# Optimization experiments

Hardware: AMD Instinct MI355X
Metric: run time of the kernel (lower is better)

## Reference

```python
import jax, jax.numpy as jnp
import numpy as np

B, S, D, E = 8, 128, 768, 100

def setup_inputs() -> dict:
    key = jax.random.key(0)
    ks = jax.random.split(key, 7)
    s = 1.0 / np.sqrt(D)  # roughly Linear init scale
    return {
        "x":     jax.random.normal(ks[0], (B, S, D), dtype=jnp.float32),
        "w_lin": jax.random.normal(ks[1], (E, D, D), dtype=jnp.float32) * s,
        "b_lin": jax.random.normal(ks[2], (E, D), dtype=jnp.float32) * s,
        "w1":    jax.random.normal(ks[3], (E, D, D), dtype=jnp.float32) * s,
        "b1":    jax.random.normal(ks[4], (E, D), dtype=jnp.float32) * s,
        "w2":    jax.random.normal(ks[5], (E, D, D), dtype=jnp.float32) * s,
        "b2":    jax.random.normal(ks[6], (E, D), dtype=jnp.float32) * s,
    }

def reference(x, w_lin, b_lin, w1, b1, w2, b2):
    # Torch Linear: y = x @ W.T + b, weights stacked over experts e.
    # Skip branch: [B,S,O,E]
    lin = jnp.einsum('bsd,eod->bsoe', x, w_lin) + b_lin.T[None, None]
    # MLP branch (dropout is identity in eval mode); exact (erf) GELU as nn.GELU default.
    h = jax.nn.gelu(jnp.einsum('bsd,ehd->bseh', x, w1) + b1[None, None], approximate=False)
    mlp = jnp.einsum('bseh,eoh->bsoe', h, w2) + b2.T[None, None]
    # torch.stack([...], dim=-1) -> [B, S, D_out, E]
    return lin + mlp
```

## Files before the change

### kernel.cpp

```cpp
#include <hip/hip_runtime.h>
#include <hip/hip_bf16.h>
#include <cstdint>

typedef __attribute__((ext_vector_type(8))) short short8;
typedef __attribute__((ext_vector_type(4))) float f32x4;
typedef unsigned short u16;
typedef unsigned int u32;

#define Mdim 1024
#define Ddim 768
#define Edim 100
#define DD (Ddim * Ddim)

__device__ __forceinline__ u16 f2bf(float f) {
  u32 u = __builtin_bit_cast(u32, f);
  u += 0x7fffu + ((u >> 16) & 1u);
  return (u16)(u >> 16);
}
__device__ __forceinline__ float bf2f(u16 h) {
  return __builtin_bit_cast(float, ((u32)h) << 16);
}
__device__ __forceinline__ u32 pack2(float a, float b) {
  return (u32)f2bf(a) | ((u32)f2bf(b) << 16);
}

__device__ __forceinline__ float gelu_f(float v) {
  float v2 = v * v;
  float wv = v * (2.30220795f + 0.10294322f * v2);
  float ew = __builtin_amdgcn_exp2f(wv);
  return v - v * __builtin_amdgcn_rcpf(ew + 1.0f);
}

#define GLL16(gsrc, ldst)                                                        \
  __builtin_amdgcn_global_load_lds(                                             \
      (const __attribute__((address_space(1))) u32*)(gsrc),                     \
      (__attribute__((address_space(3))) u32*)(ldst), 16, 0, 0)

#define VM8 asm volatile("s_waitcnt vmcnt(8)" ::: "memory")
#define VM0 asm volatile("s_waitcnt vmcnt(0)" ::: "memory")
#define LGKM0 asm volatile("s_waitcnt lgkmcnt(0)" ::: "memory")
#define RAW_BAR                                                                  \
  do {                                                                           \
    __builtin_amdgcn_s_barrier();                                                \
    asm volatile("" ::: "memory");                                               \
  } while (0)

__global__ void k_cvt(const float* __restrict__ x, u16* __restrict__ xb) {
  size_t i = ((size_t)blockIdx.x * 256 + threadIdx.x) * 4;
  float4 v = *(const float4*)(x + i);
  uint2 r;
  r.x = pack2(v.x, v.y);
  r.y = pack2(v.z, v.w);
  *(uint2*)(xb + i) = r;
}

__global__ __launch_bounds__(256) void k_cvtw(const float* __restrict__ w,
                                              u16* __restrict__ wb, int n8) {
  const int stride = gridDim.x * 256;
  for (int i = blockIdx.x * 256 + threadIdx.x; i < n8; i += stride) {
    const size_t o = (size_t)i * 8;
    const float4 f0 = *(const float4*)(w + o);
    const float4 f1 = *(const float4*)(w + o + 4);
    uint4 v;
    v.x = pack2(f0.x, f0.y); v.y = pack2(f0.z, f0.w);
    v.z = pack2(f1.x, f1.y); v.w = pack2(f1.z, f1.w);
    *(uint4*)(wb + o) = v;
  }
}

template <int NT>
__device__ __forceinline__ void gemm8(const u16* __restrict__ A0,
                                      const u16* __restrict__ A1,
                                      const u16* __restrict__ B0,
                                      const u16* __restrict__ B1,
                                      u16* lds, f32x4 (&acc)[8][4], const int t) {
  const int w = t >> 6, l = t & 63;
  const int wr = (w >> 2) << 7;
  const int wc = (w & 3) << 6;
  const int lr = l & 15, c4 = l >> 4, r7 = l & 7;
  const int sl0 = ((c4 ^ r7) << 3);
  const int sl1 = (((4 | c4) ^ r7) << 3);
  const size_t soff = (size_t)((w << 5) + (l >> 3)) * Ddim + (((l & 7) ^ (l >> 3)) << 3);

  auto stage_op = [&](const u16* src, int buf, int isB, int kk) {
    u16* d = lds + (buf << 15) + (isB << 14) + (w << 11);
    const u16* s = src + soff + (kk << 6);
#pragma unroll
    for (int i = 0; i < 4; ++i)
      GLL16(s + (size_t)(i << 3) * Ddim, d + (i << 9));
  };
  auto stage = [&](int tt, int isB) {
    const int buf = tt & 1;
    if (NT == 24 && tt >= 12) stage_op(isB ? B1 : A1, buf, isB, tt - 12);
    else                      stage_op(isB ? B0 : A0, buf, isB, tt);
  };

  short8 af[16], bf[4];
  auto rdA = [&](int buf, int half) {
    const u16* ab = lds + (buf << 15) + (wr + (half << 6) + lr) * 64;
#pragma unroll
    for (int m = 0; m < 4; ++m) {
      af[half * 8 + m * 2]     = *(const short8*)(ab + (m << 10) + sl0);
      af[half * 8 + m * 2 + 1] = *(const short8*)(ab + (m << 10) + sl1);
    }
  };
  auto rdB = [&](int buf, int half) {
    const u16* bb = lds + (buf << 15) + 16384 + (wc + (half << 5) + lr) * 64;
#pragma unroll
    for (int n = 0; n < 2; ++n) {
      bf[n * 2]     = *(const short8*)(bb + (n << 10) + sl0);
      bf[n * 2 + 1] = *(const short8*)(bb + (n << 10) + sl1);
    }
  };
  auto q = [&](int mh, int nh) {
    __builtin_amdgcn_s_setprio(1);
#pragma unroll
    for (int m = 0; m < 4; ++m)
#pragma unroll
      for (int n = 0; n < 2; ++n) {
        f32x4 c = acc[mh * 4 + m][nh * 2 + n];
        c = __builtin_amdgcn_mfma_f32_16x16x32_bf16(af[mh * 8 + m * 2],     bf[n * 2],     c, 0, 0, 0);
        c = __builtin_amdgcn_mfma_f32_16x16x32_bf16(af[mh * 8 + m * 2 + 1], bf[n * 2 + 1], c, 0, 0, 0);
        acc[mh * 4 + m][nh * 2 + n] = c;
      }
    __builtin_amdgcn_s_setprio(0);
  };

  stage(0, 1); stage(0, 0);
  stage(1, 1); stage(1, 0);
  VM8;
  RAW_BAR;

#pragma unroll 2
  for (int T = 0; T < NT - 2; ++T) {
    const int buf = T & 1;
    rdA(buf, 0); rdB(buf, 0);
    RAW_BAR; q(0, 0); RAW_BAR;
    rdA(buf, 1);
    RAW_BAR; q(1, 0); RAW_BAR;
    rdB(buf, 1); stage(T + 2, 0);
    RAW_BAR; q(1, 1); RAW_BAR;
    stage(T + 2, 1);
    VM8;
    RAW_BAR; q(0, 1); RAW_BAR;
  }
  {
    const int buf = (NT - 2) & 1;
    rdA(buf, 0); rdB(buf, 0); RAW_BAR; q(0, 0); RAW_BAR;
    rdA(buf, 1);              RAW_BAR; q(1, 0); RAW_BAR;
    rdB(buf, 1);              RAW_BAR; q(1, 1); RAW_BAR;
    VM0; RAW_BAR; q(0, 1); RAW_BAR;
  }
  {
    const int buf = (NT - 1) & 1;
    rdA(buf, 0); rdB(buf, 0); RAW_BAR; q(0, 0); RAW_BAR;
    rdA(buf, 1);              RAW_BAR; q(1, 0); RAW_BAR;
    rdB(buf, 1);              RAW_BAR; q(1, 1); RAW_BAR;
    q(0, 1);
  }
}

template <bool GELU>
__device__ __forceinline__ void epi_store(f32x4 (&acc)[8][4], const float* bias,
                                          u16* lds, u16* gout, int m_base, int n_base,
                                          const int t) {
  const int w = t >> 6, l = t & 63;
  const int lr = l & 15, c4 = l >> 4;
  u16* reg = lds + (w << 13);

  LGKM0;
  __builtin_amdgcn_sched_barrier(0);
  RAW_BAR;

  float bv[4];
#pragma unroll
  for (int nf = 0; nf < 4; ++nf) bv[nf] = bias[(nf << 4) + lr];

#pragma unroll
  for (int mf = 0; mf < 8; ++mf) {
#pragma unroll
    for (int nf = 0; nf < 4; ++nf) {
      const int slot = (nf << 1) + (lr >> 3);
      const int bis = (lr & 7);
#pragma unroll
      for (int j = 0; j < 4; ++j) {
        float v = acc[mf][nf][j] + bv[nf];
        if (GELU) v = gelu_f(v);
        const int row = (mf << 4) + (c4 << 2) + j;
        reg[row * 64 + ((slot ^ (row & 7)) << 3) + bis] = f2bf(v);
      }
    }
  }
  const int g = l >> 3;
  const int phys = ((l & 7) ^ g) << 3;
#pragma unroll
  for (int r = 0; r < 16; ++r) {
    const int row = (r << 3) + g;
    short8 v = *(const short8*)(reg + row * 64 + phys);
    *(short8*)(gout + (size_t)(m_base + row) * Ddim + n_base + ((l & 7) << 3)) = v;
  }
}

__device__ __forceinline__ void decode8(int bid, int& e, int& m0, int& n0) {
  const int s = (bid & 7) * 150 + (bid >> 3);
  e = s / 12;
  const int r = s % 12;
  m0 = (r & 3) << 8;
  n0 = (r >> 2) << 8;
}

__global__ __launch_bounds__(512, 2) void k_h6(const u16* __restrict__ xb,
                                               const u16* __restrict__ w1b,
                                               const float* __restrict__ b1,
                                               u16* __restrict__ hout) {
  __shared__ __align__(16) u16 lds[65536];
  int e, m0, n0;
  decode8(blockIdx.x, e, m0, n0);
  const int t = threadIdx.x;
  f32x4 acc[8][4] = {};
  gemm8<12>(xb + (size_t)m0 * Ddim, nullptr,
            w1b + (size_t)e * DD + (size_t)n0 * Ddim, nullptr, lds, acc, t);

  const int w = t >> 6;
  const int wr = (w >> 2) << 7, wc = (w & 3) << 6;
  epi_store<true>(acc, b1 + (size_t)e * Ddim + n0 + wc, lds,
                  hout + (size_t)e * Mdim * Ddim, m0 + wr, n0 + wc, t);
}

__global__ __launch_bounds__(512, 2) void k_out6(const u16* __restrict__ xb,
                                                 const u16* __restrict__ hbuf,
                                                 const u16* __restrict__ wlb,
                                                 const float* __restrict__ b_lin,
                                                 const u16* __restrict__ w2b,
                                                 const float* __restrict__ b2,
                                                 u16* __restrict__ tout) {
  __shared__ __align__(16) u16 lds[65536];
  int e, m0, n0;
  decode8(blockIdx.x, e, m0, n0);
  const int t = threadIdx.x;
  f32x4 acc[8][4] = {};
  gemm8<24>(xb + (size_t)m0 * Ddim,
            hbuf + (size_t)e * Mdim * Ddim + (size_t)m0 * Ddim,
            wlb + (size_t)e * DD + (size_t)n0 * Ddim,
            w2b + (size_t)e * DD + (size_t)n0 * Ddim, lds, acc, t);

  const int w = t >> 6, l = t & 63;
  const int wr = (w >> 2) << 7, wc = (w & 3) << 6;
  const int lr = l & 15;
  const float* bm = b2 + (size_t)e * Ddim + n0 + wc;
#pragma unroll
  for (int nf = 0; nf < 4; ++nf) {
    const float bmv = bm[(nf << 4) + lr];
#pragma unroll
    for (int mf = 0; mf < 8; ++mf)
#pragma unroll
      for (int j = 0; j < 4; ++j) acc[mf][nf][j] += bmv;
  }
  epi_store<false>(acc, b_lin + (size_t)e * Ddim + n0 + wc, lds,
                   tout + (size_t)e * Mdim * Ddim, m0 + wr, n0 + wc, t);
}

__global__ __launch_bounds__(256) void k_tr_bf(const u16* __restrict__ tbuf,
                                               float* __restrict__ out) {
  __shared__ __align__(16) u16 tile[100 * 260];
  const int t = threadIdx.x;
  const size_t MD = (size_t)Mdim * Ddim;
  const size_t md0 = (size_t)blockIdx.x * 256;
#pragma unroll
  for (int p = 0; p < 25; ++p) {
    const int e = p * 4 + (t >> 6);
    const int c = (t & 63) * 4;
    uint2 v = *(const uint2*)(tbuf + (size_t)e * MD + md0 + c);
    *(uint2*)(&tile[e * 260 + c]) = v;
  }
  __syncthreads();
  const size_t obase = md0 * 100;
#pragma unroll 5
  for (int i = 0; i < 100; ++i) {
    const int flat = t + i * 256;
    const int mo = (int)(((u32)flat * 5243u) >> 19);
    const int e = flat - mo * 100;
    out[obase + flat] = bf2f(tile[e * 260 + mo]);
  }
}

__device__ __forceinline__ void gemm_phase_f32(const u16* __restrict__ Ag,
                                               const float* __restrict__ Wg,
                                               u16* As, u16* Bs, f32x4 (&acc)[4][4], int t) {
  const int w = t >> 6, l = t & 63;
  const int lrow = l & 15, lk = (l >> 4) << 3;
  const int wr = ((w >> 1) << 6), wc = ((w & 1) << 6);
  for (int kt = 0; kt < Ddim; kt += 32) {
#pragma unroll
    for (int i = 0; i < 2; ++i) {
      GLL16(Ag + (size_t)((w << 5) + (i << 4) + (l >> 2)) * Ddim + kt + ((l & 3) << 3),
            As + (((w << 5) + (i << 4)) << 5));
    }
    {
      const int r = t >> 1, c = (t & 1) << 4;
      const float* src = Wg + (size_t)r * Ddim + kt + c;
      const float4 f0 = *(const float4*)(src);
      const float4 f1 = *(const float4*)(src + 4);
      const float4 f2 = *(const float4*)(src + 8);
      const float4 f3 = *(const float4*)(src + 12);
      uint4 v0, v1;
      v0.x = pack2(f0.x, f0.y); v0.y = pack2(f0.z, f0.w);
      v0.z = pack2(f1.x, f1.y); v0.w = pack2(f1.z, f1.w);
      v1.x = pack2(f2.x, f2.y); v1.y = pack2(f2.z, f2.w);
      v1.z = pack2(f3.x, f3.y); v1.w = pack2(f3.z, f3.w);
      *(uint4*)(&Bs[r * 32 + c]) = v0;
      *(uint4*)(&Bs[r * 32 + c + 8]) = v1;
    }
    __syncthreads();
    short8 af[4], bfr[4];
#pragma unroll
    for (int f = 0; f < 4; ++f) {
      af[f]  = *(const short8*)(&As[(wr + f * 16 + lrow) * 32 + lk]);
      bfr[f] = *(const short8*)(&Bs[(wc + f * 16 + lrow) * 32 + lk]);
    }
#pragma unroll
    for (int fm = 0; fm < 4; ++fm)
#pragma unroll
      for (int fn = 0; fn < 4; ++fn)
        acc[fm][fn] = __builtin_amdgcn_mfma_f32_16x16x32_bf16(af[fm], bfr[fn], acc[fm][fn], 0, 0, 0);
    __syncthreads();
  }
}

__global__ __launch_bounds__(256) void k_h2(const u16* __restrict__ xb,
                                            const float* __restrict__ w1,
                                            const float* __restrict__ b1,
                                            u16* __restrict__ hout, int e_base) {
  __shared__ __align__(16) u16 As[128 * 32];
  __shared__ __align__(16) u16 Bs[128 * 32];
  const int el = blockIdx.x / 48, r = blockIdx.x % 48;
  const int m0 = (r / 6) * 128, n0 = (r % 6) * 128;
  const int e = e_base + el;
  const int t = threadIdx.x, l = t & 63, wv = t >> 6;
  const int wr = (wv >> 1) * 64, wc = (wv & 1) * 64, lrow = l & 15;
  f32x4 acc[4][4] = {};
  gemm_phase_f32(xb + (size_t)m0 * Ddim, w1 + (size_t)e * DD + (size_t)n0 * Ddim, As, Bs, acc, t);
  const float* bias = b1 + (size_t)e * Ddim + n0;
  u16* hb = hout + (size_t)el * Mdim * Ddim;
#pragma unroll
  for (int fm = 0; fm < 4; ++fm) {
    const int mb = m0 + wr + fm * 16 + ((l >> 4) << 2);
#pragma unroll
    for (int fn = 0; fn < 4; ++fn) {
      const int nc = wc + fn * 16 + lrow;
      const float bv = bias[nc];
#pragma unroll
      for (int j = 0; j < 4; ++j) {
        float v = acc[fm][fn][j] + bv;
        v = 0.5f * v * (1.0f + erff(v * 0.7071067811865475f));
        hb[(size_t)(mb + j) * Ddim + n0 + nc] = f2bf(v);
      }
    }
  }
}

__global__ __launch_bounds__(256) void k_out2(
    const u16* __restrict__ xb, const u16* __restrict__ hbuf,
    const float* __restrict__ wl, const float* __restrict__ b_lin,
    const float* __restrict__ w2, const float* __restrict__ b2,
    float* __restrict__ out, int e_base) {
  __shared__ __align__(16) u16 As[128 * 32];
  __shared__ __align__(16) u16 Bs[128 * 32];
  const int el = blockIdx.x / 48, r = blockIdx.x % 48;
  const int m0 = (r / 6) * 128, n0 = (r % 6) * 128;
  const int e = e_base + el;
  const int t = threadIdx.x, l = t & 63, wv = t >> 6;
  const int wr = (wv >> 1) * 64, wc = (wv & 1) * 64, lrow = l & 15;
  f32x4 acc[4][4] = {};
  gemm_phase_f32(xb + (size_t)m0 * Ddim, wl + (size_t)e * DD + (size_t)n0 * Ddim, As, Bs, acc, t);
  gemm_phase_f32(hbuf + (size_t)el * Mdim * Ddim + (size_t)m0 * Ddim,
                 w2 + (size_t)e * DD + (size_t)n0 * Ddim, As, Bs, acc, t);
  const float* bl = b_lin + (size_t)e * Ddim + n0;
  const float* bm = b2 + (size_t)e * Ddim + n0;
#pragma unroll
  for (int fm = 0; fm < 4; ++fm) {
    const int mb = m0 + wr + fm * 16 + ((l >> 4) << 2);
#pragma unroll
    for (int fn = 0; fn < 4; ++fn) {
      const int nc = wc + fn * 16 + lrow;
      const float bv = bl[nc] + bm[nc];
#pragma unroll
      for (int j = 0; j < 4; ++j)
        out[((size_t)(mb + j) * Ddim + n0 + nc) * Edim + e] = acc[fm][fn][j] + bv;
    }
  }
}

extern "C" void kernel_launch(void* const* d_in, const int* in_sizes, int n_in,
                              void* d_out, int out_size, void* d_ws, size_t ws_size,
                              hipStream_t stream) {
  const float* x     = (const float*)d_in[0];
  const float* w_lin = (const float*)d_in[1];
  const float* b_lin = (const float*)d_in[2];
  const float* w1    = (const float*)d_in[3];
  const float* b1    = (const float*)d_in[4];
  const float* w2    = (const float*)d_in[5];
  const float* b2    = (const float*)d_in[6];
  float* out = (float*)d_out;

  const size_t MD = (size_t)Mdim * Ddim;
  const size_t xb_b   = MD * 2;
  const size_t w1_b   = (size_t)Edim * DD * 2;
  const size_t wreg_b = 2 * w1_b;
  const size_t h_b    = (size_t)Edim * MD * 2;
  const size_t tb_b   = h_b;
  const int NW8 = (int)((size_t)Edim * DD / 8);

  char* base = (char*)d_ws;
  u16* xb = (u16*)base;
  k_cvt<<<dim3((u32)(MD / 1024)), dim3(256), 0, stream>>>(x, xb);

  if (ws_size >= xb_b + wreg_b + h_b + tb_b) {
    u16* wreg = (u16*)(base + xb_b);
    u16* hbuf = (u16*)(base + xb_b + wreg_b);
    u16* tbuf = (u16*)(base + xb_b + wreg_b + h_b);
    k_cvtw<<<dim3(2048), dim3(256), 0, stream>>>(w1, wreg, NW8);
    k_h6<<<dim3(1200), dim3(512), 0, stream>>>(xb, wreg, b1, hbuf);
    k_cvtw<<<dim3(2048), dim3(256), 0, stream>>>(w_lin, wreg, NW8);
    k_cvtw<<<dim3(2048), dim3(256), 0, stream>>>(w2, wreg + (size_t)Edim * DD, NW8);
    k_out6<<<dim3(1200), dim3(512), 0, stream>>>(xb, hbuf, wreg, b_lin,
                                                 wreg + (size_t)Edim * DD, b2, tbuf);
    k_tr_bf<<<dim3((u32)(MD / 256)), dim3(256), 0, stream>>>(tbuf, out);
  } else {
    size_t avail = ws_size > xb_b ? ws_size - xb_b : 0;
    int EC = (int)(avail / (MD * 2));
    if (EC < 1) EC = 1;
    if (EC > Edim) EC = Edim;
    u16* hbuf = (u16*)(base + xb_b);
    for (int e0 = 0; e0 < Edim; e0 += EC) {
      int ne = (Edim - e0) < EC ? (Edim - e0) : EC;
      k_h2<<<dim3(ne * 48), dim3(256), 0, stream>>>(xb, w1, b1, hbuf, e0);
      k_out2<<<dim3(ne * 48), dim3(256), 0, stream>>>(xb, hbuf, w_lin, b_lin, w2, b2,
                                                      out, e0);
    }
  }
}
```

Before: 705.2 us.

## Fuse fp32 weight conversion into GEMM B-tile staging via register loads

Drops the separate weight-conversion kernels. The GEMMs now read fp32 weights directly: B tiles are loaded into registers, packed to bf16, and written to swizzled LDS, while A tiles still use direct global-to-LDS loads. The quarter order is also rearranged so A and B fragment registers can be reused. This removes an extra full pass over all weights (read fp32, write bf16, read bf16 again) and frees the weight workspace, at the cost of twice the global bytes per B tile inside the GEMM, higher register pressure, and B-tile LDS writes that are no longer asynchronous.

Measured after the change: 794.2 us. +12.6%, slower.

```diff
diff --git a/kernel.cpp b/kernel.cpp
--- a/kernel.cpp
+++ b/kernel.cpp
@@ -37,6 +37,7 @@
       (__attribute__((address_space(3))) u32*)(ldst), 16, 0, 0)
 
 #define VM8 asm volatile("s_waitcnt vmcnt(8)" ::: "memory")
+#define VM4 asm volatile("s_waitcnt vmcnt(4)" ::: "memory")
 #define VM0 asm volatile("s_waitcnt vmcnt(0)" ::: "memory")
 #define LGKM0 asm volatile("s_waitcnt lgkmcnt(0)" ::: "memory")
 #define RAW_BAR                                                                  \
@@ -54,109 +55,135 @@
   *(uint2*)(xb + i) = r;
 }
 
-__global__ __launch_bounds__(256) void k_cvtw(const float* __restrict__ w,
-                                              u16* __restrict__ wb, int n8) {
-  const int stride = gridDim.x * 256;
-  for (int i = blockIdx.x * 256 + threadIdx.x; i < n8; i += stride) {
-    const size_t o = (size_t)i * 8;
-    const float4 f0 = *(const float4*)(w + o);
-    const float4 f1 = *(const float4*)(w + o + 4);
-    uint4 v;
-    v.x = pack2(f0.x, f0.y); v.y = pack2(f0.z, f0.w);
-    v.z = pack2(f1.x, f1.y); v.w = pack2(f1.z, f1.w);
-    *(uint4*)(wb + o) = v;
-  }
-}
-
 template <int NT>
-__device__ __forceinline__ void gemm8(const u16* __restrict__ A0,
-                                      const u16* __restrict__ A1,
-                                      const u16* __restrict__ B0,
-                                      const u16* __restrict__ B1,
-                                      u16* lds, f32x4 (&acc)[8][4], const int t) {
+__device__ __forceinline__ void gemm8f(const u16* __restrict__ A0,
+                                       const u16* __restrict__ A1,
+                                       const float* __restrict__ B0,
+                                       const float* __restrict__ B1,
+                                       u16* lds, f32x4 (&acc)[8][4], const int t) {
   const int w = t >> 6, l = t & 63;
   const int wr = (w >> 2) << 7;
   const int wc = (w & 3) << 6;
   const int lr = l & 15, c4 = l >> 4, r7 = l & 7;
   const int sl0 = ((c4 ^ r7) << 3);
   const int sl1 = (((4 | c4) ^ r7) << 3);
-  const size_t soff = (size_t)((w << 5) + (l >> 3)) * Ddim + (((l & 7) ^ (l >> 3)) << 3);
-
-  auto stage_op = [&](const u16* src, int buf, int isB, int kk) {
-    u16* d = lds + (buf << 15) + (isB << 14) + (w << 11);
-    const u16* s = src + soff + (kk << 6);
+  const size_t soffA = (size_t)((w << 5) + (l >> 3)) * Ddim + (((l & 7) ^ (l >> 3)) << 3);
+  const size_t soffB = (size_t)((w << 5) + (l >> 3)) * Ddim + ((l & 7) << 3);
+  const int ldsB = ((w << 5) + (l >> 3)) * 64 + (((l & 7) ^ (l >> 3)) << 3);
+
+  auto stageA = [&](int tt) {
+    const u16* src = (NT == 24 && tt >= 12) ? A1 : A0;
+    const int kk = (NT == 24 && tt >= 12) ? tt - 12 : tt;
+    u16* d = lds + ((tt & 1) << 15) + (w << 11);
+    const u16* s = src + soffA + (kk << 6);
 #pragma unroll
     for (int i = 0; i < 4; ++i)
       GLL16(s + (size_t)(i << 3) * Ddim, d + (i << 9));
   };
-  auto stage = [&](int tt, int isB) {
-    const int buf = tt & 1;
-    if (NT == 24 && tt >= 12) stage_op(isB ? B1 : A1, buf, isB, tt - 12);
-    else                      stage_op(isB ? B0 : A0, buf, isB, tt);
-  };
-
-  short8 af[16], bf[4];
-  auto rdA = [&](int buf, int half) {
+  auto issueB = [&](int tt, uint4 (&br)[8]) {
+    const float* src = (NT == 24 && tt >= 12) ? B1 : B0;
+    const int kk = (NT == 24 && tt >= 12) ? tt - 12 : tt;
+    const float* s = src + soffB + (kk << 6);
+#pragma unroll
+    for (int i = 0; i < 4; ++i) {
+      br[i * 2]     = *(const uint4*)(s + (size_t)(i << 3) * Ddim);
+      br[i * 2 + 1] = *(const uint4*)(s + (size_t)(i << 3) * Ddim + 4);
+    }
+    asm volatile("" ::: "memory");
+  };
+  auto writeB = [&](int tt, uint4 (&br)[8]) {
+    u16* base = lds + ((tt & 1) << 15) + 16384 + ldsB;
+#pragma unroll
+    for (int i = 0; i < 4; ++i) {
+      const uint4 va = br[i * 2], vb = br[i * 2 + 1];
+      uint4 o;
+      o.x = pack2(__builtin_bit_cast(float, va.x), __builtin_bit_cast(float, va.y));
+      o.y = pack2(__builtin_bit_cast(float, va.z), __builtin_bit_cast(float, va.w));
+      o.z = pack2(__builtin_bit_cast(float, vb.x), __builtin_bit_cast(float, vb.y));
+      o.w = pack2(__builtin_bit_cast(float, vb.z), __builtin_bit_cast(float, vb.w));
+      *(uint4*)(base + (i << 3) * 64) = o;
+    }
+  };
+
+  auto rdA = [&](int buf, int half, short8 (&af)[8]) {
     const u16* ab = lds + (buf << 15) + (wr + (half << 6) + lr) * 64;
 #pragma unroll
     for (int m = 0; m < 4; ++m) {
-      af[half * 8 + m * 2]     = *(const short8*)(ab + (m << 10) + sl0);
-      af[half * 8 + m * 2 + 1] = *(const short8*)(ab + (m << 10) + sl1);
-    }
-  };
-  auto rdB = [&](int buf, int half) {
+      af[m * 2]     = *(const short8*)(ab + (m << 10) + sl0);
+      af[m * 2 + 1] = *(const short8*)(ab + (m << 10) + sl1);
+    }
+  };
+  auto rdB = [&](int buf, int half, short8 (&bfh)[4]) {
     const u16* bb = lds + (buf << 15) + 16384 + (wc + (half << 5) + lr) * 64;
 #pragma unroll
     for (int n = 0; n < 2; ++n) {
-      bf[n * 2]     = *(const short8*)(bb + (n << 10) + sl0);
-      bf[n * 2 + 1] = *(const short8*)(bb + (n << 10) + sl1);
-    }
-  };
-  auto q = [&](int mh, int nh) {
+      bfh[n * 2]     = *(const short8*)(bb + (n << 10) + sl0);
+      bfh[n * 2 + 1] = *(const short8*)(bb + (n << 10) + sl1);
+    }
+  };
+  auto q = [&](int mh, int nh, short8 (&af)[8], short8 (&bfh)[4]) {
     __builtin_amdgcn_s_setprio(1);
 #pragma unroll
     for (int m = 0; m < 4; ++m)
 #pragma unroll
       for (int n = 0; n < 2; ++n) {
         f32x4 c = acc[mh * 4 + m][nh * 2 + n];
-        c = __builtin_amdgcn_mfma_f32_16x16x32_bf16(af[mh * 8 + m * 2],     bf[n * 2],     c, 0, 0, 0);
-        c = __builtin_amdgcn_mfma_f32_16x16x32_bf16(af[mh * 8 + m * 2 + 1], bf[n * 2 + 1], c, 0, 0, 0);
+        c = __builtin_amdgcn_mfma_f32_16x16x32_bf16(af[m * 2],     bfh[n * 2],     c, 0, 0, 0);
+        c = __builtin_amdgcn_mfma_f32_16x16x32_bf16(af[m * 2 + 1], bfh[n * 2 + 1], c, 0, 0, 0);
         acc[mh * 4 + m][nh * 2 + n] = c;
       }
     __builtin_amdgcn_s_setprio(0);
   };
 
-  stage(0, 1); stage(0, 0);
-  stage(1, 1); stage(1, 0);
-  VM8;
-  RAW_BAR;
-
+  {
+    uint4 br0[8], br1[8];
+    issueB(0, br0); issueB(1, br1);
+    stageA(0); stageA(1);
+    VM8;
+    writeB(0, br0); writeB(1, br1);
+    VM4;
+    LGKM0;
+    RAW_BAR;
+  }
+
+  short8 afr[8], bf0[4], bf1[4];
+  uint4 br[8];
 #pragma unroll 2
   for (int T = 0; T < NT - 2; ++T) {
     const int buf = T & 1;
-    rdA(buf, 0); rdB(buf, 0);
-    RAW_BAR; q(0, 0); RAW_BAR;
-    rdA(buf, 1);
-    RAW_BAR; q(1, 0); RAW_BAR;
-    rdB(buf, 1); stage(T + 2, 0);
-    RAW_BAR; q(1, 1); RAW_BAR;
-    stage(T + 2, 1);
-    VM8;
-    RAW_BAR; q(0, 1); RAW_BAR;
+    issueB(T + 2, br);
+    rdA(buf, 0, afr); rdB(buf, 0, bf0);
+    RAW_BAR; q(0, 0, afr, bf0); RAW_BAR;
+    rdB(buf, 1, bf1);
+    RAW_BAR; q(0, 1, afr, bf1); RAW_BAR;
+    rdA(buf, 1, afr);
+    RAW_BAR; q(1, 1, afr, bf1); RAW_BAR;
+    stageA(T + 2);
+    writeB(T + 2, br);
+    VM4;
+    LGKM0;
+    RAW_BAR; q(1, 0, afr, bf0); RAW_BAR;
   }
   {
     const int buf = (NT - 2) & 1;
-    rdA(buf, 0); rdB(buf, 0); RAW_BAR; q(0, 0); RAW_BAR;
-    rdA(buf, 1);              RAW_BAR; q(1, 0); RAW_BAR;
-    rdB(buf, 1);              RAW_BAR; q(1, 1); RAW_BAR;
-    VM0; RAW_BAR; q(0, 1); RAW_BAR;
+    rdA(buf, 0, afr); rdB(buf, 0, bf0);
+    RAW_BAR; q(0, 0, afr, bf0); RAW_BAR;
+    rdB(buf, 1, bf1);
+    RAW_BAR; q(0, 1, afr, bf1); RAW_BAR;
+    rdA(buf, 1, afr);
+    RAW_BAR; q(1, 1, afr, bf1); RAW_BAR;
+    VM0;
+    RAW_BAR; q(1, 0, afr, bf0); RAW_BAR;
   }
   {
     const int buf = (NT - 1) & 1;
-    rdA(buf, 0); rdB(buf, 0); RAW_BAR; q(0, 0); RAW_BAR;
-    rdA(buf, 1);              RAW_BAR; q(1, 0); RAW_BAR;
-    rdB(buf, 1);              RAW_BAR; q(1, 1); RAW_BAR;
-    q(0, 1);
+    rdA(buf, 0, afr); rdB(buf, 0, bf0);
+    RAW_BAR; q(0, 0, afr, bf0); RAW_BAR;
+    rdB(buf, 1, bf1);
+    RAW_BAR; q(0, 1, afr, bf1); RAW_BAR;
+    rdA(buf, 1, afr);
+    RAW_BAR; q(1, 1, afr, bf1); RAW_BAR;
+    q(1, 0, afr, bf0);
   }
 }
 
@@ -209,8 +236,8 @@
   n0 = (r >> 2) << 8;
 }
 
-__global__ __launch_bounds__(512, 2) void k_h6(const u16* __restrict__ xb,
-                                               const u16* __restrict__ w1b,
+__global__ __launch_bounds__(512, 2) void k_h7(const u16* __restrict__ xb,
+                                               const float* __restrict__ w1,
                                                const float* __restrict__ b1,
                                                u16* __restrict__ hout) {
   __shared__ __align__(16) u16 lds[65536];
@@ -218,8 +245,8 @@
   decode8(blockIdx.x, e, m0, n0);
   const int t = threadIdx.x;
   f32x4 acc[8][4] = {};
-  gemm8<12>(xb + (size_t)m0 * Ddim, nullptr,
-            w1b + (size_t)e * DD + (size_t)n0 * Ddim, nullptr, lds, acc, t);
+  gemm8f<12>(xb + (size_t)m0 * Ddim, nullptr,
+             w1 + (size_t)e * DD + (size_t)n0 * Ddim, nullptr, lds, acc, t);
 
   const int w = t >> 6;
   const int wr = (w >> 2) << 7, wc = (w & 3) << 6;
@@ -227,11 +254,11 @@
                   hout + (size_t)e * Mdim * Ddim, m0 + wr, n0 + wc, t);
 }
 
-__global__ __launch_bounds__(512, 2) void k_out6(const u16* __restrict__ xb,
+__global__ __launch_bounds__(512, 2) void k_out7(const u16* __restrict__ xb,
                                                  const u16* __restrict__ hbuf,
-                                                 const u16* __restrict__ wlb,
+                                                 const float* __restrict__ wl,
                                                  const float* __restrict__ b_lin,
-                                                 const u16* __restrict__ w2b,
+                                                 const float* __restrict__ w2,
                                                  const float* __restrict__ b2,
                                                  u16* __restrict__ tout) {
   __shared__ __align__(16) u16 lds[65536];
@@ -239,10 +266,10 @@
   decode8(blockIdx.x, e, m0, n0);
   const int t = threadIdx.x;
   f32x4 acc[8][4] = {};
-  gemm8<24>(xb + (size_t)m0 * Ddim,
-            hbuf + (size_t)e * Mdim * Ddim + (size_t)m0 * Ddim,
-            wlb + (size_t)e * DD + (size_t)n0 * Ddim,
-            w2b + (size_t)e * DD + (size_t)n0 * Ddim, lds, acc, t);
+  gemm8f<24>(xb + (size_t)m0 * Ddim,
+             hbuf + (size_t)e * Mdim * Ddim + (size_t)m0 * Ddim,
+             wl + (size_t)e * DD + (size_t)n0 * Ddim,
+             w2 + (size_t)e * DD + (size_t)n0 * Ddim, lds, acc, t);
 
   const int w = t >> 6, l = t & 63;
   const int wr = (w >> 2) << 7, wc = (w & 3) << 6;
@@ -404,27 +431,19 @@
   float* out = (float*)d_out;
 
   const size_t MD = (size_t)Mdim * Ddim;
-  const size_t xb_b   = MD * 2;
-  const size_t w1_b   = (size_t)Edim * DD * 2;
-  const size_t wreg_b = 2 * w1_b;
-  const size_t h_b    = (size_t)Edim * MD * 2;
-  const size_t tb_b   = h_b;
-  const int NW8 = (int)((size_t)Edim * DD / 8);
+  const size_t xb_b = MD * 2;
+  const size_t h_b  = (size_t)Edim * MD * 2;
+  const size_t tb_b = h_b;
 
   char* base = (char*)d_ws;
   u16* xb = (u16*)base;
   k_cvt<<<dim3((u32)(MD / 1024)), dim3(256), 0, stream>>>(x, xb);
 
-  if (ws_size >= xb_b + wreg_b + h_b + tb_b) {
-    u16* wreg = (u16*)(base + xb_b);
-    u16* hbuf = (u16*)(base + xb_b + wreg_b);
-    u16* tbuf = (u16*)(base + xb_b + wreg_b + h_b);
-    k_cvtw<<<dim3(2048), dim3(256), 0, stream>>>(w1, wreg, NW8);
-    k_h6<<<dim3(1200), dim3(512), 0, stream>>>(xb, wreg, b1, hbuf);
-    k_cvtw<<<dim3(2048), dim3(256), 0, stream>>>(w_lin, wreg, NW8);
-    k_cvtw<<<dim3(2048), dim3(256), 0, stream>>>(w2, wreg + (size_t)Edim * DD, NW8);
-    k_out6<<<dim3(1200), dim3(512), 0, stream>>>(xb, hbuf, wreg, b_lin,
-                                                 wreg + (size_t)Edim * DD, b2, tbuf);
+  if (ws_size >= xb_b + h_b + tb_b) {
+    u16* hbuf = (u16*)(base + xb_b);
+    u16* tbuf = (u16*)(base + xb_b + h_b);
+    k_h7<<<dim3(1200), dim3(512), 0, stream>>>(xb, w1, b1, hbuf);
+    k_out7<<<dim3(1200), dim3(512), 0, stream>>>(xb, hbuf, w_lin, b_lin, w2, b2, tbuf);
     k_tr_bf<<<dim3((u32)(MD / 256)), dim3(256), 0, stream>>>(tbuf, out);
   } else {
     size_t avail = ws_size > xb_b ? ws_size - xb_b : 0;
```

## Fuse weight conversions into prep and first GEMM kernels to cut launches

Applied to the files above, without the earlier changes.

Merges the x and w1 bf16 conversions into a single prep kernel. It also moves the w_lin and w2 conversions into the tail of the first expert GEMM kernel, so they run inside that kernel instead of as separate launches. The aim is to drop kernel launches and let the conversion traffic overlap with GEMM tail work. The cost is a larger workspace (a third weight buffer) and GEMM blocks that run longer, with their conversion loops competing with other blocks' GEMM work for bandwidth.

After: 728.6 us. 3.3% more time.

```diff
diff --git a/kernel.cpp b/kernel.cpp
--- a/kernel.cpp
+++ b/kernel.cpp
@@ -11,6 +11,7 @@
 #define Ddim 768
 #define Edim 100
 #define DD (Ddim * Ddim)
+#define NW8 7372800
 
 __device__ __forceinline__ u16 f2bf(float f) {
   u32 u = __builtin_bit_cast(u32, f);
@@ -45,27 +46,23 @@
     asm volatile("" ::: "memory");                                               \
   } while (0)
 
-__global__ void k_cvt(const float* __restrict__ x, u16* __restrict__ xb) {
-  size_t i = ((size_t)blockIdx.x * 256 + threadIdx.x) * 4;
-  float4 v = *(const float4*)(x + i);
-  uint2 r;
-  r.x = pack2(v.x, v.y);
-  r.y = pack2(v.z, v.w);
-  *(uint2*)(xb + i) = r;
-}
-
-__global__ __launch_bounds__(256) void k_cvtw(const float* __restrict__ w,
-                                              u16* __restrict__ wb, int n8) {
-  const int stride = gridDim.x * 256;
-  for (int i = blockIdx.x * 256 + threadIdx.x; i < n8; i += stride) {
-    const size_t o = (size_t)i * 8;
-    const float4 f0 = *(const float4*)(w + o);
-    const float4 f1 = *(const float4*)(w + o + 4);
-    uint4 v;
-    v.x = pack2(f0.x, f0.y); v.y = pack2(f0.z, f0.w);
-    v.z = pack2(f1.x, f1.y); v.w = pack2(f1.z, f1.w);
-    *(uint4*)(wb + o) = v;
-  }
+__device__ __forceinline__ void cvt8(const float* __restrict__ s, u16* __restrict__ d) {
+  const float4 f0 = *(const float4*)(s);
+  const float4 f1 = *(const float4*)(s + 4);
+  uint4 v;
+  v.x = pack2(f0.x, f0.y); v.y = pack2(f0.z, f0.w);
+  v.z = pack2(f1.x, f1.y); v.w = pack2(f1.z, f1.w);
+  *(uint4*)(d) = v;
+}
+
+__global__ __launch_bounds__(256) void k_prep(const float* __restrict__ x,
+                                              u16* __restrict__ xb,
+                                              const float* __restrict__ w1,
+                                              u16* __restrict__ w1b) {
+  const int tid = blockIdx.x * 256 + threadIdx.x;
+  if (tid < (Mdim * Ddim) / 8) cvt8(x + (size_t)tid * 8, xb + (size_t)tid * 8);
+  for (int i = tid; i < NW8; i += 2048 * 256)
+    cvt8(w1 + (size_t)i * 8, w1b + (size_t)i * 8);
 }
 
 template <int NT>
@@ -209,10 +206,14 @@
   n0 = (r >> 2) << 8;
 }
 
-__global__ __launch_bounds__(512, 2) void k_h6(const u16* __restrict__ xb,
+__global__ __launch_bounds__(512, 2) void k_h8(const u16* __restrict__ xb,
                                                const u16* __restrict__ w1b,
                                                const float* __restrict__ b1,
-                                               u16* __restrict__ hout) {
+                                               u16* __restrict__ hout,
+                                               const float* __restrict__ wl,
+                                               const float* __restrict__ w2,
+                                               u16* __restrict__ wlb,
+                                               u16* __restrict__ w2b) {
   __shared__ __align__(16) u16 lds[65536];
   int e, m0, n0;
   decode8(blockIdx.x, e, m0, n0);
@@ -225,9 +226,15 @@
   const int wr = (w >> 2) << 7, wc = (w & 3) << 6;
   epi_store<true>(acc, b1 + (size_t)e * Ddim + n0 + wc, lds,
                   hout + (size_t)e * Mdim * Ddim, m0 + wr, n0 + wc, t);
-}
-
-__global__ __launch_bounds__(512, 2) void k_out6(const u16* __restrict__ xb,
+
+  const int tid = blockIdx.x * 512 + t;
+  for (int i = tid; i < NW8; i += 1200 * 512)
+    cvt8(wl + (size_t)i * 8, wlb + (size_t)i * 8);
+  for (int i = tid; i < NW8; i += 1200 * 512)
+    cvt8(w2 + (size_t)i * 8, w2b + (size_t)i * 8);
+}
+
+__global__ __launch_bounds__(512, 2) void k_out8(const u16* __restrict__ xb,
                                                  const u16* __restrict__ hbuf,
                                                  const u16* __restrict__ wlb,
                                                  const float* __restrict__ b_lin,
@@ -282,6 +289,15 @@
     const int e = flat - mo * 100;
     out[obase + flat] = bf2f(tile[e * 260 + mo]);
   }
+}
+
+__global__ void k_cvt(const float* __restrict__ x, u16* __restrict__ xb) {
+  size_t i = ((size_t)blockIdx.x * 256 + threadIdx.x) * 4;
+  float4 v = *(const float4*)(x + i);
+  uint2 r;
+  r.x = pack2(v.x, v.y);
+  r.y = pack2(v.z, v.w);
+  *(uint2*)(xb + i) = r;
 }
 
 __device__ __forceinline__ void gemm_phase_f32(const u16* __restrict__ Ag,
@@ -404,29 +420,27 @@
   float* out = (float*)d_out;
 
   const size_t MD = (size_t)Mdim * Ddim;
-  const size_t xb_b   = MD * 2;
-  const size_t w1_b   = (size_t)Edim * DD * 2;
-  const size_t wreg_b = 2 * w1_b;
-  const size_t h_b    = (size_t)Edim * MD * 2;
-  const size_t tb_b   = h_b;
-  const int NW8 = (int)((size_t)Edim * DD / 8);
+  const size_t xb_b = MD * 2;
+  const size_t w_b  = (size_t)Edim * DD * 2;
+  const size_t h_b  = (size_t)Edim * MD * 2;
+  const size_t tb_b = h_b;
 
   char* base = (char*)d_ws;
-  u16* xb = (u16*)base;
-  k_cvt<<<dim3((u32)(MD / 1024)), dim3(256), 0, stream>>>(x, xb);
-
-  if (ws_size >= xb_b + wreg_b + h_b + tb_b) {
-    u16* wreg = (u16*)(base + xb_b);
-    u16* hbuf = (u16*)(base + xb_b + wreg_b);
-    u16* tbuf = (u16*)(base + xb_b + wreg_b + h_b);
-    k_cvtw<<<dim3(2048), dim3(256), 0, stream>>>(w1, wreg, NW8);
-    k_h6<<<dim3(1200), dim3(512), 0, stream>>>(xb, wreg, b1, hbuf);
-    k_cvtw<<<dim3(2048), dim3(256), 0, stream>>>(w_lin, wreg, NW8);
-    k_cvtw<<<dim3(2048), dim3(256), 0, stream>>>(w2, wreg + (size_t)Edim * DD, NW8);
-    k_out6<<<dim3(1200), dim3(512), 0, stream>>>(xb, hbuf, wreg, b_lin,
-                                                 wreg + (size_t)Edim * DD, b2, tbuf);
+
+  if (ws_size >= xb_b + 3 * w_b + h_b + tb_b) {
+    u16* xb   = (u16*)base;
+    u16* w1b  = (u16*)(base + xb_b);
+    u16* wlb  = (u16*)(base + xb_b + w_b);
+    u16* w2b  = (u16*)(base + xb_b + 2 * w_b);
+    u16* hbuf = (u16*)(base + xb_b + 3 * w_b);
+    u16* tbuf = (u16*)(base + xb_b + 3 * w_b + h_b);
+    k_prep<<<dim3(2048), dim3(256), 0, stream>>>(x, xb, w1, w1b);
+    k_h8<<<dim3(1200), dim3(512), 0, stream>>>(xb, w1b, b1, hbuf, w_lin, w2, wlb, w2b);
+    k_out8<<<dim3(1200), dim3(512), 0, stream>>>(xb, hbuf, wlb, b_lin, w2b, b2, tbuf);
     k_tr_bf<<<dim3((u32)(MD / 256)), dim3(256), 0, stream>>>(tbuf, out);
   } else {
+    u16* xb = (u16*)base;
+    k_cvt<<<dim3((u32)(MD / 1024)), dim3(256), 0, stream>>>(x, xb);
     size_t avail = ws_size > xb_b ? ws_size - xb_b : 0;
     int EC = (int)(avail / (MD * 2));
     if (EC < 1) EC = 1;
```
